# Kernel optimization log

Hardware: AMD Instinct MI355X
Metric: run time of the kernel (lower is better)

Reference implementation:

```python
import jax, jax.numpy as jnp
import numpy as np

S, A = 8, 2
SA = S + A
N = 256


def setup_inputs() -> dict:
    key = jax.random.key(0)
    ks = jax.random.split(key, 8)
    mean_full = jax.random.normal(ks[0], (SA,), dtype=jnp.float32)
    C = jax.random.normal(ks[1], (SA, SA), dtype=jnp.float32)
    cov_full = (C @ C.T) / SA + 0.1 * jnp.eye(SA, dtype=jnp.float32)  # PSD input covariance
    dynamics_inputs = jax.random.normal(ks[2], (N, SA), dtype=jnp.float32)
    dynamics_outputs = jax.random.normal(ks[3], (N, S), dtype=jnp.float32)
    eq_coeff = 0.5 + 0.5 * jax.random.uniform(ks[4], (S,), dtype=jnp.float32)
    eq_scales = 0.5 + 0.5 * jax.random.uniform(ks[5], (S, SA), dtype=jnp.float32)
    eq_noise_coeff = 1e-2 + 1e-2 * jax.random.uniform(ks[6], (S,), dtype=jnp.float32)
    return {
        'mean_full': mean_full,
        'cov_full': cov_full,
        'dynamics_inputs': dynamics_inputs,
        'dynamics_outputs': dynamics_outputs,
        'eq_coeff': eq_coeff,
        'eq_scales': eq_scales,
        'eq_noise_coeff': eq_noise_coeff,
    }


def _eq_kernel_log(x, x_, eq_coeff, eq_scales):
    # x: [n, d], x_: [m, d] -> [S, n, m] log kernel
    diffs = x[:, None, :] - x_[None, :, :]
    quads = jnp.einsum('nmd,nmd,gd->gnm', diffs, diffs, 1.0 / eq_scales)
    return jnp.log(eq_coeff)[:, None, None] - 0.5 * quads


def reference(mean_full, cov_full, dynamics_inputs, dynamics_outputs,
              eq_coeff, eq_scales, eq_noise_coeff):
    s_dim = eq_coeff.shape[0]
    sa = mean_full.shape[0]
    n = dynamics_inputs.shape[0]
    dtype = mean_full.dtype
    mean_full = mean_full.reshape(1, sa)
    cov_full = cov_full.reshape(sa, sa)
    inv_scales = 1.0 / eq_scales  # [S, SA]
    eye_sa = jnp.eye(sa, dtype=dtype)

    # data covariance K + noise: [S, N, N]
    log_K = _eq_kernel_log(dynamics_inputs, dynamics_inputs, eq_coeff, eq_scales)
    data_cov = jnp.exp(log_K) + eq_noise_coeff[:, None, None] * eye_sa[None, :n, :n] if n == sa else jnp.exp(log_K) + eq_noise_coeff[:, None, None] * jnp.eye(n, dtype=dtype)[None]
    # beta: [S, N]
    beta = jnp.linalg.solve(data_cov, dynamics_outputs.T[:, :, None])[:, :, 0]

    # mean determinant coefficient: det(cov_full diag(1/scales_g) + I)^(-1/2)
    M = cov_full[None, :, :] * inv_scales[:, None, :] + eye_sa[None]  # [S, SA, SA]
    mean_det_coeff = eq_coeff * jnp.linalg.det(M) ** (-0.5)  # [S]

    cov_full_plus_scales = cov_full[None] + jax.vmap(jnp.diag)(eq_scales)  # [S, SA, SA]
    nu = dynamics_inputs - mean_full  # [N, SA]
    sol = jnp.linalg.solve(cov_full_plus_scales,
                           jnp.broadcast_to(nu.T[None], (s_dim, sa, n)))  # [S, SA, N]
    mean_quad = jnp.einsum('id,gdi->gi', nu, sol)
    mean_exp_quad = mean_det_coeff[:, None] * jnp.exp(-0.5 * mean_quad)  # [S, N]
    mean = jnp.einsum('gi,gi->g', beta, mean_exp_quad)  # [S]

    # R_ab = cov_full (inv_a + inv_b) + I: [S, S, SA, SA]
    cross = inv_scales[:, None, :] + inv_scales[None, :, :]  # [S, S, SA]
    R = cov_full[None, None, :, :] * cross[:, :, None, :] + eye_sa[None, None]
    _, log_R_det = jnp.linalg.slogdet(R)
    log_R_det_inv_sqrt = -0.5 * log_R_det  # [S, S]

    log_k_data_mu = _eq_kernel_log(mean_full, dynamics_inputs, eq_coeff, eq_scales)  # [S, 1, N]
    log_k_ab = log_k_data_mu[None, :, :, :] + log_k_data_mu[:, :, :, None]  # [S, S, N, N]

    eq_scale_times_nu = nu[None, :, :] * inv_scales[:, None, :]  # [S, N, SA]
    z = (eq_scale_times_nu[:, None, :, None, :] +
         eq_scale_times_nu[None, :, None, :, :])  # [S, S, N, N, SA]
    # R^{-1} cov_full, then quadratic form z^T (R^{-1} cov_full) z
    R_inv = jnp.linalg.inv(R)  # [S, S, SA, SA]
    M_ab = jnp.einsum('abij,jk->abik', R_inv, cov_full)  # [S, S, SA, SA]
    cov_quad = 0.5 * jnp.einsum('abnmi,abij,abnmj->abnm', z, M_ab, z)

    log_Q = log_k_ab + cov_quad + log_R_det_inv_sqrt[:, :, None, None]
    Q = jnp.exp(log_Q)  # [S, S, N, N]

    Q_diag = Q[jnp.arange(s_dim), jnp.arange(s_dim)]  # [S, N, N]
    expected_var = eq_coeff - jnp.trace(jnp.linalg.solve(data_cov, Q_diag),
                                        axis1=-2, axis2=-1)  # [S]

    cov = jnp.einsum('ai,bj,abij->ab', beta, beta, Q)
    cov = cov - mean[:, None] * mean[None, :]
    cov = cov + jnp.diag(expected_var)

    # input-output cross covariance
    A_inv_mean = jnp.linalg.solve(cov_full_plus_scales,
                                  jnp.broadcast_to(mean_full.T[None], (s_dim, sa, 1)))  # [S, SA, 1]
    A_inv_dyn = jnp.linalg.solve(cov_full_plus_scales,
                                 jnp.broadcast_to(dynamics_inputs.T[None], (s_dim, sa, n)))  # [S, SA, N]
    cross_cov_mu = eq_scales[:, :, None] * A_inv_mean + jnp.einsum('ij,gjk->gik', cov_full, A_inv_dyn)
    cross_cov = jnp.einsum('gk,gdk,gk->dg', mean_exp_quad, cross_cov_mu, beta)  # [SA, S]
    cross_cov_s = cross_cov[:s_dim, :] - mean_full[:, :s_dim].T * mean[None, :]

    mean = mean + mean_full[0, :s_dim]
    cov = cov + cov_full[:s_dim, :s_dim]
    cov = cov + cross_cov_s + cross_cov_s.T
    return mean, cov
```

## Files before the change

kernel.cpp:

```cpp
#include <hip/hip_runtime.h>
#include <math.h>

#define S_DIM 8
#define SA_DIM 10
#define NN 256

constexpr size_t OFF_K     = 0;
constexpr size_t OFF_LINV  = OFF_K    + 8ull*NN*NN;
constexpr size_t OFF_KINV  = OFF_LINV + 8ull*NN*NN;
constexpr size_t OFF_RD    = OFF_KINV + 8ull*NN*NN;
constexpr size_t OFF_U     = OFF_RD   + 8*NN;
constexpr size_t OFF_LK    = OFF_U    + 8*NN*SA_DIM;
constexpr size_t OFF_M     = OFF_LK   + 8*NN;
constexpr size_t OFF_C     = OFF_M    + 64*100;
constexpr size_t OFF_AINV  = OFF_C    + 64;
constexpr size_t OFF_AIM   = OFF_AINV + 800;
constexpr size_t OFF_MDC   = OFF_AIM  + 80;
constexpr size_t OFF_BETA  = OFF_MDC  + 8;
constexpr size_t OFF_MEAN  = OFF_BETA + 8*NN;
constexpr size_t OFF_CROSS = OFF_MEAN + 8;
constexpr size_t OFF_COVP  = OFF_CROSS+ 80;
constexpr size_t OFF_TRP   = OFF_COVP + 512;

__device__ void gj_invert10(float A[SA_DIM][SA_DIM], float B[SA_DIM][SA_DIM], float* logdet) {
#pragma unroll
  for (int i = 0; i < SA_DIM; i++)
#pragma unroll
    for (int j = 0; j < SA_DIM; j++) B[i][j] = (i == j) ? 1.f : 0.f;
  float ld = 0.f;
#pragma unroll
  for (int k = 0; k < SA_DIM; k++) {
    float pv = A[k][k];
    ld += logf(pv);
    float ip = 1.f / pv;
#pragma unroll
    for (int j = 0; j < SA_DIM; j++) { A[k][j] *= ip; B[k][j] *= ip; }
#pragma unroll
    for (int r = 0; r < SA_DIM; r++) {
      if (r == k) continue;
      float f = A[r][k];
#pragma unroll
      for (int j = 0; j < SA_DIM; j++) { A[r][j] -= f * A[k][j]; B[r][j] -= f * B[k][j]; }
    }
  }
  *logdet = ld;
}

__global__ __launch_bounds__(256) void k_front(const float* __restrict__ x,
                                               const float* __restrict__ mf,
                                               const float* __restrict__ cov,
                                               const float* __restrict__ eqc,
                                               const float* __restrict__ scales,
                                               const float* __restrict__ noise,
                                               float* __restrict__ Kw,
                                               float* __restrict__ u,
                                               float* __restrict__ lkw,
                                               float* __restrict__ Mw, float* __restrict__ cvec,
                                               float* __restrict__ Ainvw, float* __restrict__ aimw,
                                               float* __restrict__ mdcw) {
  int blk = blockIdx.x;
  if (blk < 2048) {
    int g = blk >> 8;
    int n = blk & 255;
    int m = threadIdx.x;
    __shared__ float xs[NN * SA_DIM];
    __shared__ float isc[SA_DIM];
    for (int i = threadIdx.x; i < NN * SA_DIM; i += 256) xs[i] = x[i];
    if (threadIdx.x < SA_DIM) isc[threadIdx.x] = 1.0f / scales[g * SA_DIM + threadIdx.x];
    __syncthreads();
    float quad = 0.f;
#pragma unroll
    for (int d = 0; d < SA_DIM; d++) {
      float df = xs[n * SA_DIM + d] - xs[m * SA_DIM + d];
      quad += df * df * isc[d];
    }
    float v = eqc[g] * __expf(-0.5f * quad);
    if (m == n) v += noise[g];
    Kw[(size_t)g * NN * NN + (size_t)n * NN + m] = v;
  } else if (blk < 2056) {
    int g = blk - 2048;
    int n = threadIdx.x;
    float quad = 0.f;
#pragma unroll
    for (int d = 0; d < SA_DIM; d++) {
      float isc = 1.0f / scales[g * SA_DIM + d];
      float nu = x[n * SA_DIM + d] - mf[d];
      u[((size_t)g * NN + n) * SA_DIM + d] = nu * isc;
      quad += nu * nu * isc;
    }
    lkw[g * NN + n] = logf(eqc[g]) - 0.5f * quad;
  } else {
    int p = threadIdx.x;
    if (p >= 64) return;
    int a = p >> 3, b = p & 7;
    float A[SA_DIM][SA_DIM], B[SA_DIM][SA_DIM];
    for (int i = 0; i < SA_DIM; i++)
      for (int j = 0; j < SA_DIM; j++)
        A[i][j] = cov[i * SA_DIM + j] * (1.f / scales[a * SA_DIM + j] + 1.f / scales[b * SA_DIM + j]) +
                  ((i == j) ? 1.f : 0.f);
    float ld;
    gj_invert10(A, B, &ld);
    cvec[p] = -0.5f * ld;
    for (int i = 0; i < SA_DIM; i++)
      for (int j = 0; j < SA_DIM; j++) {
        float v = 0.f;
        for (int k = 0; k < SA_DIM; k++) v += B[i][k] * cov[k * SA_DIM + j];
        Mw[p * 100 + i * SA_DIM + j] = v;
      }
    if (b == 0) {
      int g = a;
      for (int i = 0; i < SA_DIM; i++)
        for (int j = 0; j < SA_DIM; j++)
          A[i][j] = cov[i * SA_DIM + j] + ((i == j) ? scales[g * SA_DIM + j] : 0.f);
      float ld2;
      gj_invert10(A, B, &ld2);
      for (int i = 0; i < SA_DIM; i++)
        for (int j = 0; j < SA_DIM; j++) Ainvw[g * 100 + i * SA_DIM + j] = B[i][j];
      for (int i = 0; i < SA_DIM; i++) {
        float v = 0.f;
        for (int j = 0; j < SA_DIM; j++) v += B[i][j] * mf[j];
        aimw[g * SA_DIM + i] = v;
      }
      for (int i = 0; i < SA_DIM; i++)
        for (int j = 0; j < SA_DIM; j++)
          A[i][j] = cov[i * SA_DIM + j] * (1.f / scales[g * SA_DIM + j]) + ((i == j) ? 1.f : 0.f);
      float ld3;
      gj_invert10(A, B, &ld3);
      mdcw[g] = eqc[g] * __expf(-0.5f * ld3);
    }
  }
}

__device__ __forceinline__ void tile_idx(int tau, int ntile, int nt4, int c0,
                                         int& ib, int& jb, int& iq, int& jq) {
  int rt = ntile - 1 - tau;
  int q = (int)((sqrtf((float)(8 * rt + 1)) - 1.0f) * 0.5f);
  while ((q + 1) * (q + 2) / 2 <= rt) q++;
  while (q * (q + 1) / 2 > rt) q--;
  jq = nt4 - 1 - q;
  int rem = rt - q * (q + 1) / 2;
  iq = nt4 - 1 - rem;
  jb = c0 + 16 + 4 * jq;
  ib = c0 + 16 + 4 * iq;
}

__device__ __forceinline__ void chol_factor_panel(float* __restrict__ Ag,
                                                  float* __restrict__ rdg,
                                                  int c0, int nb, int t, int lane,
                                                  bool fromGlobal,
                                                  const float (*SRC)[248],
                                                  float (*Pdst)[248]) {
  int rr = lane & 15;
  float a[16];
  float myrs = 0.f;
  if (fromGlobal) {
#pragma unroll
    for (int j = 0; j < 16; j++)
      a[j] = (j <= rr) ? Ag[(size_t)(c0 + j) * NN + (c0 + rr)]
                       : Ag[(size_t)(c0 + rr) * NN + (c0 + j)];
  } else {
#pragma unroll
    for (int j = 0; j < 16; j++)
      a[j] = (j <= rr) ? SRC[j][rr] : SRC[rr][j];
  }
#pragma unroll
  for (int k = 0; k < 16; k++) {
    float d = __shfl(a[k], k);
    float rs_ = rsqrtf(d);
    if (rr == k) myrs = rs_;
    float m = a[k] * rs_;
#pragma unroll
    for (int j = 0; j < 16; j++) {
      if (j > k) {
        float Lkj = __shfl(a[j], k) * rs_;
        a[j] = fmaf(-m, Lkj, a[j]);
      }
    }
    a[k] = m;
  }
  if (t < 16) {
    rdg[c0 + rr] = myrs;
#pragma unroll
    for (int j = 0; j < 16; j++)
      if (j <= rr) Ag[(size_t)(c0 + j) * NN + (c0 + rr)] = a[j];
  }
  if (t < nb) {
    int i = c0 + 16 + t;
    (void)i;
    float xs[16];
#pragma unroll
    for (int c = 0; c < 16; c++) {
      float x = fromGlobal ? Ag[(size_t)(c0 + c) * NN + (c0 + 16 + t)] : SRC[c][16 + t];
#pragma unroll
      for (int cp = 0; cp < 16; cp++) {
        if (cp < c) {
          float Lccp = __shfl(a[cp], c);
          x = fmaf(-Lccp, xs[cp], x);
        }
      }
      xs[c] = x * __shfl(myrs, c);
    }
#pragma unroll
    for (int c = 0; c < 16; c++)
      Pdst[c][t] = xs[c];
  }
}

__global__ __launch_bounds__(1024, 4) void k_chol13(float* __restrict__ Aw,
                                                    float* __restrict__ rd) {
  int g = blockIdx.x;
  float* Ag = Aw + (size_t)g * NN * NN;
  float* rdg = rd + g * NN;
  int t = threadIdx.x;
  int lane = t & 63;
  int w = t >> 6;
  __shared__ __align__(16) float P[2][16][248];
  __shared__ __align__(16) float NP[16][248];

  if (w < 4)
    chol_factor_panel(Ag, rdg, 0, 240, t, lane, true, nullptr, P[0]);
  __syncthreads();

  for (int p = 0; p < 15; p++) {
    int c0 = 16 * p;
    int nb = NN - c0 - 16;
    int nt4 = nb >> 2;
    const float (*Pc)[248] = P[p & 1];
    int ncrit = 4 * nt4 - 6;
    if (t < ncrit) {
      int jq, iq;
      if (t < nt4) { jq = 0; iq = t; }
      else if (t < 2 * nt4 - 1) { jq = 1; iq = t - nt4 + 1; }
      else if (t < 3 * nt4 - 3) { jq = 2; iq = t - (2 * nt4 - 1) + 2; }
      else { jq = 3; iq = t - (3 * nt4 - 3) + 3; }
      int jb = c0 + 16 + 4 * jq, ib = c0 + 16 + 4 * iq;
      float4 cv0 = *(const float4*)(Ag + (size_t)(jb + 0) * NN + ib);
      float4 cv1 = *(const float4*)(Ag + (size_t)(jb + 1) * NN + ib);
      float4 cv2 = *(const float4*)(Ag + (size_t)(jb + 2) * NN + ib);
      float4 cv3 = *(const float4*)(Ag + (size_t)(jb + 3) * NN + ib);
      float4 a0 = make_float4(0.f, 0.f, 0.f, 0.f), a1 = a0, a2 = a0, a3 = a0;
#pragma unroll
      for (int k = 0; k < 16; k++) {
        float4 pi = *(const float4*)(&Pc[k][4 * iq]);
        float4 pj = *(const float4*)(&Pc[k][4 * jq]);
        a0.x = fmaf(pj.x, pi.x, a0.x); a0.y = fmaf(pj.x, pi.y, a0.y);
        a0.z = fmaf(pj.x, pi.z, a0.z); a0.w = fmaf(pj.x, pi.w, a0.w);
        a1.x = fmaf(pj.y, pi.x, a1.x); a1.y = fmaf(pj.y, pi.y, a1.y);
        a1.z = fmaf(pj.y, pi.z, a1.z); a1.w = fmaf(pj.y, pi.w, a1.w);
        a2.x = fmaf(pj.z, pi.x, a2.x); a2.y = fmaf(pj.z, pi.y, a2.y);
        a2.z = fmaf(pj.z, pi.z, a2.z); a2.w = fmaf(pj.z, pi.w, a2.w);
        a3.x = fmaf(pj.w, pi.x, a3.x); a3.y = fmaf(pj.w, pi.y, a3.y);
        a3.z = fmaf(pj.w, pi.z, a3.z); a3.w = fmaf(pj.w, pi.w, a3.w);
      }
      cv0.x -= a0.x; cv0.y -= a0.y; cv0.z -= a0.z; cv0.w -= a0.w;
      cv1.x -= a1.x; cv1.y -= a1.y; cv1.z -= a1.z; cv1.w -= a1.w;
      cv2.x -= a2.x; cv2.y -= a2.y; cv2.z -= a2.z; cv2.w -= a2.w;
      cv3.x -= a3.x; cv3.y -= a3.y; cv3.z -= a3.z; cv3.w -= a3.w;
      *(float4*)(&NP[4 * jq + 0][4 * iq]) = cv0;
      *(float4*)(&NP[4 * jq + 1][4 * iq]) = cv1;
      *(float4*)(&NP[4 * jq + 2][4 * iq]) = cv2;
      *(float4*)(&NP[4 * jq + 3][4 * iq]) = cv3;
    }
    {
      int nb4 = nb >> 2;
      int tot = 16 * nb4;
      for (int e = t; e < tot; e += 1024) {
        int c = e / nb4, s4 = e - c * nb4;
        float4 v = *(const float4*)(&Pc[c][4 * s4]);
        *(float4*)(Ag + (size_t)(c0 + c) * NN + c0 + 16 + 4 * s4) = v;
      }
    }
    __syncthreads();
    if (w < 4) {
      chol_factor_panel(Ag, rdg, c0 + 16, nb - 16, t, lane, false, NP, P[(p + 1) & 1]);
    } else {
      int nt4b = nt4 - 4;
      int ntileB = nt4b * (nt4b + 1) / 2;
      int tau = t - 256;
      if (tau < ntileB) {
        int ib, jb, iq, jq;
        tile_idx(tau, ntileB, nt4b, c0 + 16, ib, jb, iq, jq);
        float4 cv0 = *(const float4*)(Ag + (size_t)(jb + 0) * NN + ib);
        float4 cv1 = *(const float4*)(Ag + (size_t)(jb + 1) * NN + ib);
        float4 cv2 = *(const float4*)(Ag + (size_t)(jb + 2) * NN + ib);
        float4 cv3 = *(const float4*)(Ag + (size_t)(jb + 3) * NN + ib);
        while (true) {
          int tau2 = tau + 768;
          bool h2 = tau2 < ntileB;
          int ib2 = 0, jb2 = 0, iq2 = 0, jq2 = 0;
          float4 n0, n1, n2, n3;
          if (h2) {
            tile_idx(tau2, ntileB, nt4b, c0 + 16, ib2, jb2, iq2, jq2);
            n0 = *(const float4*)(Ag + (size_t)(jb2 + 0) * NN + ib2);
            n1 = *(const float4*)(Ag + (size_t)(jb2 + 1) * NN + ib2);
            n2 = *(const float4*)(Ag + (size_t)(jb2 + 2) * NN + ib2);
            n3 = *(const float4*)(Ag + (size_t)(jb2 + 3) * NN + ib2);
          }
          float4 a0 = make_float4(0.f, 0.f, 0.f, 0.f), a1 = a0, a2 = a0, a3 = a0;
#pragma unroll
          for (int k = 0; k < 16; k++) {
            float4 pi = *(const float4*)(&Pc[k][16 + 4 * iq]);
            float4 pj = *(const float4*)(&Pc[k][16 + 4 * jq]);
            a0.x = fmaf(pj.x, pi.x, a0.x); a0.y = fmaf(pj.x, pi.y, a0.y);
            a0.z = fmaf(pj.x, pi.z, a0.z); a0.w = fmaf(pj.x, pi.w, a0.w);
            a1.x = fmaf(pj.y, pi.x, a1.x); a1.y = fmaf(pj.y, pi.y, a1.y);
            a1.z = fmaf(pj.y, pi.z, a1.z); a1.w = fmaf(pj.y, pi.w, a1.w);
            a2.x = fmaf(pj.z, pi.x, a2.x); a2.y = fmaf(pj.z, pi.y, a2.y);
            a2.z = fmaf(pj.z, pi.z, a2.z); a2.w = fmaf(pj.z, pi.w, a2.w);
            a3.x = fmaf(pj.w, pi.x, a3.x); a3.y = fmaf(pj.w, pi.y, a3.y);
            a3.z = fmaf(pj.w, pi.z, a3.z); a3.w = fmaf(pj.w, pi.w, a3.w);
          }
          cv0.x -= a0.x; cv0.y -= a0.y; cv0.z -= a0.z; cv0.w -= a0.w;
          cv1.x -= a1.x; cv1.y -= a1.y; cv1.z -= a1.z; cv1.w -= a1.w;
          cv2.x -= a2.x; cv2.y -= a2.y; cv2.z -= a2.z; cv2.w -= a2.w;
          cv3.x -= a3.x; cv3.y -= a3.y; cv3.z -= a3.z; cv3.w -= a3.w;
          *(float4*)(Ag + (size_t)(jb + 0) * NN + ib) = cv0;
          *(float4*)(Ag + (size_t)(jb + 1) * NN + ib) = cv1;
          *(float4*)(Ag + (size_t)(jb + 2) * NN + ib) = cv2;
          *(float4*)(Ag + (size_t)(jb + 3) * NN + ib) = cv3;
          if (!h2) break;
          tau = tau2; ib = ib2; jb = jb2; iq = iq2; jq = jq2;
          cv0 = n0; cv1 = n1; cv2 = n2; cv3 = n3;
        }
      }
    }
    __syncthreads();
  }
}

__global__ __launch_bounds__(256) void k_linv2(const float* __restrict__ LT,
                                               const float* __restrict__ rd,
                                               float* __restrict__ Linv) {
  int g = blockIdx.x >> 2;
  int q = blockIdx.x & 3;
  int w = threadIdx.x >> 6;
  int lane = threadIdx.x & 63;
  int j = 4 * q + w;
  const float* Ag = LT + (size_t)g * NN * NN;
  const float* rdg = rd + g * NN;
  float* Og = Linv + (size_t)g * NN * NN;
  __shared__ __align__(16) float Xl[4][16][16][16];
  __shared__ __align__(16) float Dv[16][16][16];
  int r = lane & 15, cq = lane >> 4;

  for (int s = 0; s < 4; s++) {
    int i = w + 4 * s;
    for (int e = lane; e < 256; e += 64) {
      int k = e >> 4, rr = e & 15;
      Xl[w][s][k][rr] = Ag[(size_t)(16 * i + k) * NN + 16 * i + rr];
    }
    asm volatile("s_waitcnt lgkmcnt(0)" ::: "memory");
    __builtin_amdgcn_sched_barrier(0);
    int c = lane & 15;
    float xv[16];
#pragma unroll
    for (int rr = 0; rr < 16; rr++) {
      float tmp = (rr == c) ? 1.f : 0.f;
#pragma unroll
      for (int m = 0; m < 16; m++) {
        if (m < rr) tmp = fmaf(-Xl[w][s][m][rr], xv[m], tmp);
      }
      xv[rr] = tmp * rdg[16 * i + rr];
    }
    if (lane < 16) {
#pragma unroll
      for (int rr = 0; rr < 16; rr++) Dv[i][rr][lane] = xv[rr];
    }
  }
  __syncthreads();

  {
    float4 dj = *(const float4*)&Dv[j][r][4 * cq];
    *(float4*)&Xl[w][j][r][4 * cq] = dj;
    *(float4*)(Og + (size_t)(16 * j + r) * NN + 16 * j + 4 * cq) = dj;
    float4 z = make_float4(0.f, 0.f, 0.f, 0.f);
    for (int i2 = 0; i2 < j; i2++)
      *(float4*)(Og + (size_t)(16 * i2 + r) * NN + 16 * j + 4 * cq) = z;
  }
  asm volatile("s_waitcnt lgkmcnt(0)" ::: "memory");
  __builtin_amdgcn_sched_barrier(0);

  for (int i = j + 1; i < 16; i++) {
    float4 acc = make_float4(0.f, 0.f, 0.f, 0.f);
    for (int k = j; k < i; k++) {
      const float* Lbase = Ag + (size_t)(16 * k) * NN + 16 * i + r;
      const float* Xk = &Xl[w][k][0][4 * cq];
#pragma unroll
      for (int m = 0; m < 16; m++) {
        float lv = Lbase[(size_t)m * NN];
        float4 xvv = *(const float4*)(Xk + 16 * m);
        acc.x = fmaf(lv, xvv.x, acc.x);
        acc.y = fmaf(lv, xvv.y, acc.y);
        acc.z = fmaf(lv, xvv.z, acc.z);
        acc.w = fmaf(lv, xvv.w, acc.w);
      }
    }
    float4 o = make_float4(0.f, 0.f, 0.f, 0.f);
#pragma unroll
    for (int m = 0; m < 16; m++) {
      float d = Dv[i][r][m];
      float sx = __shfl(acc.x, m + 16 * cq);
      float sy = __shfl(acc.y, m + 16 * cq);
      float sz = __shfl(acc.z, m + 16 * cq);
      float sw = __shfl(acc.w, m + 16 * cq);
      o.x = fmaf(-d, sx, o.x);
      o.y = fmaf(-d, sy, o.y);
      o.z = fmaf(-d, sz, o.z);
      o.w = fmaf(-d, sw, o.w);
    }
    *(float4*)&Xl[w][i][r][4 * cq] = o;
    *(float4*)(Og + (size_t)(16 * i + r) * NN + 16 * j + 4 * cq) = o;
    asm volatile("s_waitcnt lgkmcnt(0)" ::: "memory");
    __builtin_amdgcn_sched_barrier(0);
  }
}

__global__ __launch_bounds__(256) void k_syrk2(const float* __restrict__ Linv,
                                               float* __restrict__ Kinv) {
  int g = blockIdx.x / 10;
  int tile = blockIdx.x - g * 10;
  int ti = 0, rem = tile;
  while (rem >= 4 - ti) { rem -= 4 - ti; ti++; }
  int tj = ti + rem;
  int i0 = ti * 64, j0 = tj * 64;
  const float* A = Linv + (size_t)g * NN * NN;
  float* O = Kinv + (size_t)g * NN * NN;
  __shared__ __align__(16) float smem[4096];
  float* sa = smem;
  float* sb = smem + 2048;
  int tx = threadIdx.x & 15, ty = threadIdx.x >> 4;
  float acc[4][4] = {{0.f}};
  for (int k0 = 0; k0 < NN; k0 += 32) {
    for (int e = threadIdx.x; e < 2048; e += 256) {
      int kk = e >> 6, cc = e & 63;
      sa[kk * 64 + cc] = A[(size_t)(k0 + kk) * NN + i0 + cc];
      sb[kk * 64 + cc] = A[(size_t)(k0 + kk) * NN + j0 + cc];
    }
    __syncthreads();
#pragma unroll 8
    for (int kk = 0; kk < 32; kk++) {
      float4 av = *(const float4*)(&sa[kk * 64 + ty * 4]);
      float4 bv = *(const float4*)(&sb[kk * 64 + tx * 4]);
      acc[0][0] = fmaf(av.x, bv.x, acc[0][0]); acc[0][1] = fmaf(av.x, bv.y, acc[0][1]);
      acc[0][2] = fmaf(av.x, bv.z, acc[0][2]); acc[0][3] = fmaf(av.x, bv.w, acc[0][3]);
      acc[1][0] = fmaf(av.y, bv.x, acc[1][0]); acc[1][1] = fmaf(av.y, bv.y, acc[1][1]);
      acc[1][2] = fmaf(av.y, bv.z, acc[1][2]); acc[1][3] = fmaf(av.y, bv.w, acc[1][3]);
      acc[2][0] = fmaf(av.z, bv.x, acc[2][0]); acc[2][1] = fmaf(av.z, bv.y, acc[2][1]);
      acc[2][2] = fmaf(av.z, bv.z, acc[2][2]); acc[2][3] = fmaf(av.z, bv.w, acc[2][3]);
      acc[3][0] = fmaf(av.w, bv.x, acc[3][0]); acc[3][1] = fmaf(av.w, bv.y, acc[3][1]);
      acc[3][2] = fmaf(av.w, bv.z, acc[3][2]); acc[3][3] = fmaf(av.w, bv.w, acc[3][3]);
    }
    __syncthreads();
  }
#pragma unroll
  for (int q = 0; q < 4; q++)
#pragma unroll
    for (int r = 0; r < 4; r++)
      O[(size_t)(i0 + ty * 4 + q) * NN + j0 + tx * 4 + r] = acc[q][r];
  if (ti != tj) {
    __syncthreads();
#pragma unroll
    for (int q = 0; q < 4; q++)
#pragma unroll
      for (int r = 0; r < 4; r++)
        smem[(ty * 4 + q) * 64 + tx * 4 + r] = acc[q][r];
    __syncthreads();
    for (int e = threadIdx.x; e < 1024; e += 256) {
      int rr = e >> 4, c4 = (e & 15) * 4;
      float4 v = make_float4(smem[(c4 + 0) * 64 + rr], smem[(c4 + 1) * 64 + rr],
                             smem[(c4 + 2) * 64 + rr], smem[(c4 + 3) * 64 + rr]);
      *(float4*)(O + (size_t)(j0 + rr) * NN + i0 + c4) = v;
    }
  }
}

__global__ __launch_bounds__(256) void k_beta(const float* __restrict__ Kinv,
                                              const float* __restrict__ y,
                                              float* __restrict__ betaw) {
  int g = blockIdx.x, n = threadIdx.x;
  __shared__ __align__(16) float ys[NN];
  ys[n] = y[n * S_DIM + g];
  __syncthreads();
  const float4* Kg = (const float4*)(Kinv + (size_t)g * NN * NN + (size_t)n * NN);
  float acc = 0.f;
  for (int m4 = 0; m4 < 64; m4++) {
    float4 kv = Kg[m4];
    float4 yv = ((const float4*)ys)[m4];
    acc += kv.x * yv.x + kv.y * yv.y + kv.z * yv.z + kv.w * yv.w;
  }
  betaw[g * NN + n] = acc;
}

__global__ __launch_bounds__(256) void k_back(const float* __restrict__ u,
                                              const float* __restrict__ lkw,
                                              const float* __restrict__ Mw,
                                              const float* __restrict__ cvec,
                                              const float* __restrict__ Kinv,
                                              const float* __restrict__ betaw,
                                              const float* __restrict__ x,
                                              const float* __restrict__ mf,
                                              const float* __restrict__ cov,
                                              const float* __restrict__ scales,
                                              const float* __restrict__ Ainvw,
                                              const float* __restrict__ aimw,
                                              const float* __restrict__ mdcw,
                                              float* __restrict__ covp, float* __restrict__ trp,
                                              float* __restrict__ meanw, float* __restrict__ crossw) {
  int blk = blockIdx.x;
  int t = threadIdx.x;
  if (blk < 512) {
    int p = blk >> 3;
    int eighth = blk & 7;
    int a = p >> 3, b = p & 7;
    __shared__ __align__(16) float ub[NN * 12];
    __shared__ float Ms[100];
    __shared__ float sbv[NN];
    __shared__ float eb[NN];
    __shared__ float red[256];
    {
      const float* ur = u + (size_t)b * NN * SA_DIM + (size_t)t * SA_DIM;
      float* ud = &ub[t * 12];
#pragma unroll
      for (int d = 0; d < SA_DIM; d++) ud[d] = ur[d];
    }
    if (t < 100) Ms[t] = Mw[p * 100 + t];
    eb[t] = betaw[b * NN + t];
    __syncthreads();
    {
      const float* um = &ub[t * 12];
      float qd = 0.f;
#pragma unroll
      for (int d = 0; d < SA_DIM; d++) {
        float v = 0.f;
#pragma unroll
        for (int e = 0; e < SA_DIM; e++) v += Ms[d * SA_DIM + e] * um[e];
        qd += v * um[d];
      }
      sbv[t] = lkw[b * NN + t] + 0.5f * qd;
    }
    __syncthreads();
    int n = eighth * 32 + (t >> 3);
    int c = t & 7;
    float ua[SA_DIM];
#pragma unroll
    for (int d = 0; d < SA_DIM; d++) ua[d] = u[((size_t)a * NN + n) * SA_DIM + d];
    float va[SA_DIM];
#pragma unroll
    for (int d = 0; d < SA_DIM; d++) {
      float v = 0.f;
#pragma unroll
      for (int e = 0; e < SA_DIM; e++) v += Ms[d * SA_DIM + e] * ua[e];
      va[d] = v;
    }
    float qa = 0.f;
#pragma unroll
    for (int d = 0; d < SA_DIM; d++) qa += va[d] * ua[d];
    float pa = lkw[a * NN + n] + 0.5f * qa + cvec[p];
    float wa = betaw[a * NN + n];
    const float* Krow = Kinv + (size_t)a * NN * NN + (size_t)n * NN;
    float covacc = 0.f, tracc = 0.f;
    bool dg = (a == b);
    for (int ii = 0; ii < 32; ii++) {
      int mm = c + 8 * ii;
      const float* ur = &ub[mm * 12];
      float4 f0 = *(const float4*)ur;
      float4 f1 = *(const float4*)(ur + 4);
      float4 f2 = *(const float4*)(ur + 8);
      float s = pa + sbv[mm];
      s += va[0] * f0.x + va[1] * f0.y + va[2] * f0.z + va[3] * f0.w;
      s += va[4] * f1.x + va[5] * f1.y + va[6] * f1.z + va[7] * f1.w;
      s += va[8] * f2.x + va[9] * f2.y;
      float e = __expf(s);
      covacc += eb[mm] * e;
      if (dg) tracc += Krow[mm] * e;
    }
    covacc *= wa;
    red[t] = covacc;
    __syncthreads();
    for (int st = 128; st > 0; st >>= 1) {
      if (t < st) red[t] += red[t + st];
      __syncthreads();
    }
    if (t == 0) covp[blk] = red[0];
    if (dg) {
      red[t] = tracc;
      __syncthreads();
      for (int st = 128; st > 0; st >>= 1) {
        if (t < st) red[t] += red[t + st];
        __syncthreads();
      }
      if (t == 0) trp[a * 8 + eighth] = red[0];
    }
  } else {
    int g = blk - 512;
    int i = t;
    __shared__ float Ai[100], cv[100], aims[SA_DIM], sc[SA_DIM], mfs[SA_DIM];
    __shared__ float red[256];
    if (i < 100) { Ai[i] = Ainvw[g * 100 + i]; cv[i] = cov[i]; }
    if (i < SA_DIM) { aims[i] = aimw[g * SA_DIM + i]; sc[i] = scales[g * SA_DIM + i]; mfs[i] = mf[i]; }
    __syncthreads();
    float bg = betaw[g * NN + i];
    float xi[SA_DIM], nu[SA_DIM];
#pragma unroll
    for (int d = 0; d < SA_DIM; d++) { xi[d] = x[i * SA_DIM + d]; nu[d] = xi[d] - mfs[d]; }
    float sv[SA_DIM], ad[SA_DIM];
#pragma unroll
    for (int d = 0; d < SA_DIM; d++) {
      float s1 = 0.f, s2 = 0.f;
#pragma unroll
      for (int e = 0; e < SA_DIM; e++) { s1 += Ai[d * SA_DIM + e] * nu[e]; s2 += Ai[d * SA_DIM + e] * xi[e]; }
      sv[d] = s1;
      ad[d] = s2;
    }
    float mq = 0.f;
#pragma unroll
    for (int d = 0; d < SA_DIM; d++) mq += nu[d] * sv[d];
    float mexp = mdcw[g] * __expf(-0.5f * mq);
    float cm = bg * mexp;
    float contrib[SA_DIM];
#pragma unroll
    for (int d = 0; d < SA_DIM; d++) {
      float ccm = sc[d] * aims[d];
#pragma unroll
      for (int jj = 0; jj < SA_DIM; jj++) ccm += cv[d * SA_DIM + jj] * ad[jj];
      contrib[d] = mexp * ccm * bg;
    }
    red[i] = cm;
    __syncthreads();
    for (int st = 128; st > 0; st >>= 1) {
      if (i < st) red[i] += red[i + st];
      __syncthreads();
    }
    if (i == 0) meanw[g] = red[0];
    for (int d = 0; d < SA_DIM; d++) {
      __syncthreads();
      red[i] = contrib[d];
      __syncthreads();
      for (int st = 128; st > 0; st >>= 1) {
        if (i < st) red[i] += red[i + st];
        __syncthreads();
      }
      if (i == 0) crossw[d * S_DIM + g] = red[0];
    }
  }
}

__global__ __launch_bounds__(64) void k_final(const float* __restrict__ covp,
                                              const float* __restrict__ trp,
                                              const float* __restrict__ meanw,
                                              const float* __restrict__ crossw,
                                              const float* __restrict__ cov,
                                              const float* __restrict__ eqc,
                                              const float* __restrict__ mf,
                                              float* __restrict__ out) {
  int p = threadIdx.x;
  if (p >= 64) return;
  int a = p >> 3, b = p & 7;
  float covq = 0.f;
#pragma unroll
  for (int e = 0; e < 8; e++) covq += covp[p * 8 + e];
  float ma = meanw[a], mb = meanw[b];
  float val = covq - ma * mb + cov[a * SA_DIM + b];
  if (a == b) {
    float tr = 0.f;
#pragma unroll
    for (int e = 0; e < 8; e++) tr += trp[a * 8 + e];
    val += eqc[a] - tr;
  }
  val += (crossw[a * S_DIM + b] - mf[a] * mb) + (crossw[b * S_DIM + a] - mf[b] * ma);
  out[S_DIM + p] = val;
  if (p < S_DIM) out[p] = meanw[p] + mf[p];
}

extern "C" void kernel_launch(void* const* d_in, const int* in_sizes, int n_in,
                              void* d_out, int out_size, void* d_ws, size_t ws_size,
                              hipStream_t stream) {
  const float* mf     = (const float*)d_in[0];
  const float* cov    = (const float*)d_in[1];
  const float* x      = (const float*)d_in[2];
  const float* y      = (const float*)d_in[3];
  const float* eqc    = (const float*)d_in[4];
  const float* scales = (const float*)d_in[5];
  const float* noise  = (const float*)d_in[6];
  float* ws = (float*)d_ws;

  float* Kw    = ws + OFF_K;
  float* Linv  = ws + OFF_LINV;
  float* Kinv  = ws + OFF_KINV;
  float* rd    = ws + OFF_RD;
  float* u     = ws + OFF_U;
  float* lkw   = ws + OFF_LK;
  float* Mw    = ws + OFF_M;
  float* cvec  = ws + OFF_C;
  float* Ainvw = ws + OFF_AINV;
  float* aimw  = ws + OFF_AIM;
  float* mdcw  = ws + OFF_MDC;
  float* betaw = ws + OFF_BETA;
  float* meanw = ws + OFF_MEAN;
  float* crossw= ws + OFF_CROSS;
  float* covp  = ws + OFF_COVP;
  float* trp   = ws + OFF_TRP;

  k_front<<<2057, 256, 0, stream>>>(x, mf, cov, eqc, scales, noise, Kw, u, lkw, Mw, cvec,
                                    Ainvw, aimw, mdcw);
  k_chol13<<<8, 1024, 0, stream>>>(Kw, rd);
  k_linv2<<<32, 256, 0, stream>>>(Kw, rd, Linv);
  k_syrk2<<<80, 256, 0, stream>>>(Linv, Kinv);
  k_beta<<<8, 256, 0, stream>>>(Kinv, y, betaw);
  k_back<<<520, 256, 0, stream>>>(u, lkw, Mw, cvec, Kinv, betaw, x, mf, cov, scales,
                                  Ainvw, aimw, mdcw, covp, trp, meanw, crossw);
  k_final<<<1, 64, 0, stream>>>(covp, trp, meanw, crossw, cov, eqc, mf, (float*)d_out);
}
```

Baseline: 275.9 us.

## Fuse kernel-matrix construction into the Cholesky kernel and simplify panel writeback

Building the 8 NxN kernel matrices moves from a 2048-block front kernel into the Cholesky kernel, so each of the 8 blocks fills its own matrix before factoring. k_front shrinks to 9 blocks for the small side computations. The panel solve now writes results straight to global memory, which removes the separate cooperative copy-out loop. The software-pipelined prefetch in the trailing update becomes a plain strided loop. The fused matrix build runs on only 8 blocks of 1024 threads instead of being spread across the GPU, so that part becomes much less parallel in exchange for one fewer large launch and one fewer global round-trip.

```diff
diff --git a/kernel.cpp b/kernel.cpp
--- a/kernel.cpp
+++ b/kernel.cpp
@@ -46,39 +46,19 @@
   *logdet = ld;
 }
 
-__global__ __launch_bounds__(256) void k_front(const float* __restrict__ x,
-                                               const float* __restrict__ mf,
-                                               const float* __restrict__ cov,
-                                               const float* __restrict__ eqc,
-                                               const float* __restrict__ scales,
-                                               const float* __restrict__ noise,
-                                               float* __restrict__ Kw,
-                                               float* __restrict__ u,
-                                               float* __restrict__ lkw,
-                                               float* __restrict__ Mw, float* __restrict__ cvec,
-                                               float* __restrict__ Ainvw, float* __restrict__ aimw,
-                                               float* __restrict__ mdcw) {
+__global__ __launch_bounds__(256) void k_front9(const float* __restrict__ x,
+                                                const float* __restrict__ mf,
+                                                const float* __restrict__ cov,
+                                                const float* __restrict__ eqc,
+                                                const float* __restrict__ scales,
+                                                float* __restrict__ u,
+                                                float* __restrict__ lkw,
+                                                float* __restrict__ Mw, float* __restrict__ cvec,
+                                                float* __restrict__ Ainvw, float* __restrict__ aimw,
+                                                float* __restrict__ mdcw) {
   int blk = blockIdx.x;
-  if (blk < 2048) {
-    int g = blk >> 8;
-    int n = blk & 255;
-    int m = threadIdx.x;
-    __shared__ float xs[NN * SA_DIM];
-    __shared__ float isc[SA_DIM];
-    for (int i = threadIdx.x; i < NN * SA_DIM; i += 256) xs[i] = x[i];
-    if (threadIdx.x < SA_DIM) isc[threadIdx.x] = 1.0f / scales[g * SA_DIM + threadIdx.x];
-    __syncthreads();
-    float quad = 0.f;
-#pragma unroll
-    for (int d = 0; d < SA_DIM; d++) {
-      float df = xs[n * SA_DIM + d] - xs[m * SA_DIM + d];
-      quad += df * df * isc[d];
-    }
-    float v = eqc[g] * __expf(-0.5f * quad);
-    if (m == n) v += noise[g];
-    Kw[(size_t)g * NN * NN + (size_t)n * NN + m] = v;
-  } else if (blk < 2056) {
-    int g = blk - 2048;
+  if (blk < 8) {
+    int g = blk;
     int n = threadIdx.x;
     float quad = 0.f;
 #pragma unroll
@@ -186,11 +166,10 @@
   }
   if (t < nb) {
     int i = c0 + 16 + t;
-    (void)i;
     float xs[16];
 #pragma unroll
     for (int c = 0; c < 16; c++) {
-      float x = fromGlobal ? Ag[(size_t)(c0 + c) * NN + (c0 + 16 + t)] : SRC[c][16 + t];
+      float x = fromGlobal ? Ag[(size_t)(c0 + c) * NN + i] : SRC[c][16 + t];
 #pragma unroll
       for (int cp = 0; cp < 16; cp++) {
         if (cp < c) {
@@ -201,13 +180,19 @@
       xs[c] = x * __shfl(myrs, c);
     }
 #pragma unroll
-    for (int c = 0; c < 16; c++)
+    for (int c = 0; c < 16; c++) {
+      Ag[(size_t)(c0 + c) * NN + i] = xs[c];
       Pdst[c][t] = xs[c];
-  }
-}
-
-__global__ __launch_bounds__(1024, 4) void k_chol13(float* __restrict__ Aw,
-                                                    float* __restrict__ rd) {
+    }
+  }
+}
+
+__global__ __launch_bounds__(1024, 4) void k_cholK(const float* __restrict__ x,
+                                                   const float* __restrict__ eqc,
+                                                   const float* __restrict__ scales,
+                                                   const float* __restrict__ noise,
+                                                   float* __restrict__ Aw,
+                                                   float* __restrict__ rd) {
   int g = blockIdx.x;
   float* Ag = Aw + (size_t)g * NN * NN;
   float* rdg = rd + g * NN;
@@ -216,6 +201,28 @@
   int w = t >> 6;
   __shared__ __align__(16) float P[2][16][248];
   __shared__ __align__(16) float NP[16][248];
+  __shared__ float iscs[16];
+
+  {
+    float* xs = &NP[0][0];
+    for (int i = t; i < NN * SA_DIM; i += 1024) xs[i] = x[i];
+    if (t < SA_DIM) iscs[t] = 1.0f / scales[g * SA_DIM + t];
+    __syncthreads();
+    float eq = eqc[g], nz = noise[g];
+    for (int e = t; e < NN * NN; e += 1024) {
+      int n = e >> 8, m = e & 255;
+      float quad = 0.f;
+#pragma unroll
+      for (int d = 0; d < SA_DIM; d++) {
+        float df = xs[n * SA_DIM + d] - xs[m * SA_DIM + d];
+        quad += df * df * iscs[d];
+      }
+      float v = eq * __expf(-0.5f * quad);
+      if (n == m) v += nz;
+      Ag[e] = v;
+    }
+    __syncthreads();
+  }
 
   if (w < 4)
     chol_factor_panel(Ag, rdg, 0, 240, t, lane, true, nullptr, P[0]);
@@ -261,67 +268,41 @@
       *(float4*)(&NP[4 * jq + 2][4 * iq]) = cv2;
       *(float4*)(&NP[4 * jq + 3][4 * iq]) = cv3;
     }
-    {
-      int nb4 = nb >> 2;
-      int tot = 16 * nb4;
-      for (int e = t; e < tot; e += 1024) {
-        int c = e / nb4, s4 = e - c * nb4;
-        float4 v = *(const float4*)(&Pc[c][4 * s4]);
-        *(float4*)(Ag + (size_t)(c0 + c) * NN + c0 + 16 + 4 * s4) = v;
-      }
-    }
     __syncthreads();
     if (w < 4) {
       chol_factor_panel(Ag, rdg, c0 + 16, nb - 16, t, lane, false, NP, P[(p + 1) & 1]);
     } else {
       int nt4b = nt4 - 4;
       int ntileB = nt4b * (nt4b + 1) / 2;
-      int tau = t - 256;
-      if (tau < ntileB) {
+      for (int tau = t - 256; tau < ntileB; tau += 768) {
         int ib, jb, iq, jq;
         tile_idx(tau, ntileB, nt4b, c0 + 16, ib, jb, iq, jq);
         float4 cv0 = *(const float4*)(Ag + (size_t)(jb + 0) * NN + ib);
         float4 cv1 = *(const float4*)(Ag + (size_t)(jb + 1) * NN + ib);
         float4 cv2 = *(const float4*)(Ag + (size_t)(jb + 2) * NN + ib);
         float4 cv3 = *(const float4*)(Ag + (size_t)(jb + 3) * NN + ib);
-        while (true) {
-          int tau2 = tau + 768;
-          bool h2 = tau2 < ntileB;
-          int ib2 = 0, jb2 = 0, iq2 = 0, jq2 = 0;
-          float4 n0, n1, n2, n3;
-          if (h2) {
-            tile_idx(tau2, ntileB, nt4b, c0 + 16, ib2, jb2, iq2, jq2);
-            n0 = *(const float4*)(Ag + (size_t)(jb2 + 0) * NN + ib2);
-            n1 = *(const float4*)(Ag + (size_t)(jb2 + 1) * NN + ib2);
-            n2 = *(const float4*)(Ag + (size_t)(jb2 + 2) * NN + ib2);
-            n3 = *(const float4*)(Ag + (size_t)(jb2 + 3) * NN + ib2);
-          }
-          float4 a0 = make_float4(0.f, 0.f, 0.f, 0.f), a1 = a0, a2 = a0, a3 = a0;
-#pragma unroll
-          for (int k = 0; k < 16; k++) {
-            float4 pi = *(const float4*)(&Pc[k][16 + 4 * iq]);
-            float4 pj = *(const float4*)(&Pc[k][16 + 4 * jq]);
-            a0.x = fmaf(pj.x, pi.x, a0.x); a0.y = fmaf(pj.x, pi.y, a0.y);
-            a0.z = fmaf(pj.x, pi.z, a0.z); a0.w = fmaf(pj.x, pi.w, a0.w);
-            a1.x = fmaf(pj.y, pi.x, a1.x); a1.y = fmaf(pj.y, pi.y, a1.y);
-            a1.z = fmaf(pj.y, pi.z, a1.z); a1.w = fmaf(pj.y, pi.w, a1.w);
-            a2.x = fmaf(pj.z, pi.x, a2.x); a2.y = fmaf(pj.z, pi.y, a2.y);
-            a2.z = fmaf(pj.z, pi.z, a2.z); a2.w = fmaf(pj.z, pi.w, a2.w);
-            a3.x = fmaf(pj.w, pi.x, a3.x); a3.y = fmaf(pj.w, pi.y, a3.y);
-            a3.z = fmaf(pj.w, pi.z, a3.z); a3.w = fmaf(pj.w, pi.w, a3.w);
-          }
-          cv0.x -= a0.x; cv0.y -= a0.y; cv0.z -= a0.z; cv0.w -= a0.w;
-          cv1.x -= a1.x; cv1.y -= a1.y; cv1.z -= a1.z; cv1.w -= a1.w;
-          cv2.x -= a2.x; cv2.y -= a2.y; cv2.z -= a2.z; cv2.w -= a2.w;
-          cv3.x -= a3.x; cv3.y -= a3.y; cv3.z -= a3.z; cv3.w -= a3.w;
-          *(float4*)(Ag + (size_t)(jb + 0) * NN + ib) = cv0;
-          *(float4*)(Ag + (size_t)(jb + 1) * NN + ib) = cv1;
-          *(float4*)(Ag + (size_t)(jb + 2) * NN + ib) = cv2;
-          *(float4*)(Ag + (size_t)(jb + 3) * NN + ib) = cv3;
-          if (!h2) break;
-          tau = tau2; ib = ib2; jb = jb2; iq = iq2; jq = jq2;
-          cv0 = n0; cv1 = n1; cv2 = n2; cv3 = n3;
+        float4 a0 = make_float4(0.f, 0.f, 0.f, 0.f), a1 = a0, a2 = a0, a3 = a0;
+#pragma unroll
+        for (int k = 0; k < 16; k++) {
+          float4 pi = *(const float4*)(&Pc[k][16 + 4 * iq]);
+          float4 pj = *(const float4*)(&Pc[k][16 + 4 * jq]);
+          a0.x = fmaf(pj.x, pi.x, a0.x); a0.y = fmaf(pj.x, pi.y, a0.y);
+          a0.z = fmaf(pj.x, pi.z, a0.z); a0.w = fmaf(pj.x, pi.w, a0.w);
+          a1.x = fmaf(pj.y, pi.x, a1.x); a1.y = fmaf(pj.y, pi.y, a1.y);
+          a1.z = fmaf(pj.y, pi.z, a1.z); a1.w = fmaf(pj.y, pi.w, a1.w);
+          a2.x = fmaf(pj.z, pi.x, a2.x); a2.y = fmaf(pj.z, pi.y, a2.y);
+          a2.z = fmaf(pj.z, pi.z, a2.z); a2.w = fmaf(pj.z, pi.w, a2.w);
+          a3.x = fmaf(pj.w, pi.x, a3.x); a3.y = fmaf(pj.w, pi.y, a3.y);
+          a3.z = fmaf(pj.w, pi.z, a3.z); a3.w = fmaf(pj.w, pi.w, a3.w);
         }
+        cv0.x -= a0.x; cv0.y -= a0.y; cv0.z -= a0.z; cv0.w -= a0.w;
+        cv1.x -= a1.x; cv1.y -= a1.y; cv1.z -= a1.z; cv1.w -= a1.w;
+        cv2.x -= a2.x; cv2.y -= a2.y; cv2.z -= a2.z; cv2.w -= a2.w;
+        cv3.x -= a3.x; cv3.y -= a3.y; cv3.z -= a3.z; cv3.w -= a3.w;
+        *(float4*)(Ag + (size_t)(jb + 0) * NN + ib) = cv0;
+        *(float4*)(Ag + (size_t)(jb + 1) * NN + ib) = cv1;
+        *(float4*)(Ag + (size_t)(jb + 2) * NN + ib) = cv2;
+        *(float4*)(Ag + (size_t)(jb + 3) * NN + ib) = cv3;
       }
     }
     __syncthreads();
@@ -701,9 +682,9 @@
   float* covp  = ws + OFF_COVP;
   float* trp   = ws + OFF_TRP;
 
-  k_front<<<2057, 256, 0, stream>>>(x, mf, cov, eqc, scales, noise, Kw, u, lkw, Mw, cvec,
-                                    Ainvw, aimw, mdcw);
-  k_chol13<<<8, 1024, 0, stream>>>(Kw, rd);
+  k_front9<<<9, 256, 0, stream>>>(x, mf, cov, eqc, scales, u, lkw, Mw, cvec,
+                                  Ainvw, aimw, mdcw);
+  k_cholK<<<8, 1024, 0, stream>>>(x, eqc, scales, noise, Kw, rd);
   k_linv2<<<32, 256, 0, stream>>>(Kw, rd, Linv);
   k_syrk2<<<80, 256, 0, stream>>>(Linv, Kinv);
   k_beta<<<8, 256, 0, stream>>>(Kinv, y, betaw);
```

New measurement: 279.4 us. Within noise of the previous version (+1.3%).
